# Kernel optimization log

Measured on AMD Instinct MI355X. Metric: run time of the kernel, lower is better.

Reference implementation:

```python
import jax, jax.numpy as jnp
import numpy as np

B, S, D = 4, 2048, 1024
H = 4096          # adapter hidden dim
E = 4             # number of adapters / experts


def setup_inputs() -> dict:
    key = jax.random.key(0)
    ks = jax.random.split(key, 7)
    sd = 1.0 / np.sqrt(D)
    sh = 1.0 / np.sqrt(H)
    return {
        "x":  jax.random.normal(ks[0], (B, S, D), dtype=jnp.float32),
        "Wr": jax.random.uniform(ks[1], (D, E), minval=-sd, maxval=sd, dtype=jnp.float32),
        "br": jax.random.uniform(ks[2], (E,), minval=-sd, maxval=sd, dtype=jnp.float32),
        "W1": jax.random.uniform(ks[3], (E, D, H), minval=-sd, maxval=sd, dtype=jnp.float32),
        "b1": jax.random.uniform(ks[4], (E, H), minval=-sd, maxval=sd, dtype=jnp.float32),
        "W2": jax.random.uniform(ks[5], (E, H, D), minval=-sh, maxval=sh, dtype=jnp.float32),
        "b2": jax.random.uniform(ks[6], (E, D), minval=-sh, maxval=sh, dtype=jnp.float32),
    }


def reference(x, Wr, br, W1, b1, W2, b2):
    # Flatten tokens: (N, D)
    xf = x.reshape(-1, D)
    N = xf.shape[0]

    # Top-1 router (route_type='none' -> router input is x itself)
    logits = xf @ Wr + br                      # (N, E)
    probs = jax.nn.softmax(logits, axis=-1)    # (N, E)
    gate_idx = jnp.argmax(probs, axis=-1)      # (N,) int
    gate_val = jnp.max(probs, axis=-1)         # (N,)

    # Run every expert adapter densely (E small), then select per token.
    h = jnp.einsum('nd,edh->enh', xf, W1) + b1[:, None, :]   # (E, N, H)
    h = jax.nn.silu(h)
    eo = jnp.einsum('enh,ehd->end', h, W2) + b2[:, None, :]  # (E, N, D)

    sel = eo[gate_idx, jnp.arange(N)]          # (N, D) per-token expert output
    out = sel * gate_val[:, None]              # is_scale_prob=True scaling
    return out.reshape(B, S, D)
```

## Files before the change

kernel.cpp:

```cpp
#include <hip/hip_runtime.h>

#define DN 8192
#define DD 1024
#define DH 4096
#define DE 4
#define SLOTS (DN + 512)

typedef unsigned short u16;
typedef float f32x4 __attribute__((ext_vector_type(4)));
typedef __bf16 bf16x8 __attribute__((ext_vector_type(8)));
typedef u16 u16x2 __attribute__((ext_vector_type(2)));
typedef u16 u16x4 __attribute__((ext_vector_type(4)));

__device__ __forceinline__ u16 f2b(float f) {
  union { float f; unsigned u; } v; v.f = f;
  return (u16)((v.u + 0x7FFFu + ((v.u >> 16) & 1u)) >> 16);
}

__device__ __forceinline__ void gl_lds16(const u16* g, u16* l) {
  __builtin_amdgcn_global_load_lds((const __attribute__((address_space(1))) void*)g,
                                   (__attribute__((address_space(3))) void*)l, 16, 0, 0);
}

__global__ __launch_bounds__(256) void router_k(const float* __restrict__ x,
    const float* __restrict__ Wr, const float* __restrict__ br,
    float* __restrict__ gval, int* __restrict__ gidx, int* __restrict__ gpos,
    int* __restrict__ counts, u16* __restrict__ xb)
{
  const int tid = blockIdx.x * 256 + threadIdx.x;
  const int n = tid >> 6, lane = tid & 63;
  const float* xr = x + (size_t)n * DD;
  double a0 = 0., a1 = 0., a2 = 0., a3 = 0.;
#pragma unroll
  for (int k = 0; k < DD / 64; ++k) {
    const int d = lane + k * 64;
    const float xv = xr[d];
    const f32x4 w = *(const f32x4*)&Wr[d * 4];
    a0 += (double)xv * w[0]; a1 += (double)xv * w[1];
    a2 += (double)xv * w[2]; a3 += (double)xv * w[3];
    xb[(size_t)n * DD + d] = f2b(xv);
  }
#pragma unroll
  for (int off = 32; off; off >>= 1) {
    a0 += __shfl_xor(a0, off);
    a1 += __shfl_xor(a1, off);
    a2 += __shfl_xor(a2, off);
    a3 += __shfl_xor(a3, off);
  }
  if (lane == 0) {
    const double l0 = a0 + br[0], l1 = a1 + br[1], l2 = a2 + br[2], l3 = a3 + br[3];
    int bi = 0; double bm = l0;
    if (l1 > bm) { bm = l1; bi = 1; }
    if (l2 > bm) { bm = l2; bi = 2; }
    if (l3 > bm) { bm = l3; bi = 3; }
    const float s = __expf((float)(l0 - bm)) + __expf((float)(l1 - bm)) +
                    __expf((float)(l2 - bm)) + __expf((float)(l3 - bm));
    gval[n] = 1.0f / s;
    gidx[n] = bi;
    gpos[n] = atomicAdd(&counts[bi], 1);
  }
}

__global__ void offsets_k(const int* __restrict__ counts, int* __restrict__ offs) {
  if (threadIdx.x == 0 && blockIdx.x == 0) {
    int o = 0;
#pragma unroll
    for (int e = 0; e < DE; ++e) { offs[e] = o; o += (counts[e] + 127) & ~127; }
    offs[DE] = o;
  }
}

__global__ __launch_bounds__(256) void scatter_k(const int* __restrict__ gidx,
    const int* __restrict__ gpos, const int* __restrict__ offs, int* __restrict__ tlist) {
  const int n = blockIdx.x * 256 + threadIdx.x;
  tlist[offs[gidx[n]] + gpos[n]] = n;
}

__global__ __launch_bounds__(256) void transpose_conv(const float* __restrict__ in,
    u16* __restrict__ out, int R, int C)
{
  __shared__ u16 t[64][66];
  const int r0 = blockIdx.x * 64, c0 = blockIdx.y * 64;
  const size_t mo = (size_t)blockIdx.z * R * C;
  const int tid = threadIdx.x;
  const int i = tid >> 4, j0 = (tid & 15) * 4;
#pragma unroll
  for (int k = 0; k < 4; ++k) {
    const int row = k * 16 + i;
    const f32x4 v = *(const f32x4*)&in[mo + (size_t)(r0 + row) * C + c0 + j0];
    u16x2 u01; u01[0] = f2b(v[0]); u01[1] = f2b(v[1]);
    u16x2 u23; u23[0] = f2b(v[2]); u23[1] = f2b(v[3]);
    *(u16x2*)&t[row][j0] = u01;
    *(u16x2*)&t[row][j0 + 2] = u23;
  }
  __syncthreads();
#pragma unroll
  for (int k = 0; k < 4; ++k) {
    const int p = k * 16 + i;
    u16x4 u;
    u[0] = t[j0 + 0][p]; u[1] = t[j0 + 1][p]; u[2] = t[j0 + 2][p]; u[3] = t[j0 + 3][p];
    *(u16x4*)&out[mo + (size_t)(c0 + p) * R + r0 + j0] = u;
  }
}

#define STAGE(ks, B) do { \
    gl_lds16(pa0 + (size_t)(ks) * 32, &As[B][wid][0][0]); \
    gl_lds16(pa1 + (size_t)(ks) * 32, &As[B][wid][64][0]); \
    gl_lds16(pb0 + (size_t)(ks) * 32, &Bs[B][wid][0][0]); \
    gl_lds16(pb1 + (size_t)(ks) * 32, &Bs[B][wid][64][0]); \
  } while (0)

#define COMPUTE(B) do { \
    bf16x8 af[4], bfv[4]; \
    _Pragma("unroll") \
    for (int m = 0; m < 4; ++m) af[m] = *(const bf16x8*)&As[B][fq][wr + m * 16 + fr][0]; \
    _Pragma("unroll") \
    for (int n = 0; n < 4; ++n) bfv[n] = *(const bf16x8*)&Bs[B][fq][wc + n * 16 + fr][0]; \
    _Pragma("unroll") \
    for (int m = 0; m < 4; ++m) \
      _Pragma("unroll") \
      for (int n = 0; n < 4; ++n) \
        acc[m][n] = __builtin_amdgcn_mfma_f32_16x16x32_bf16(af[m], bfv[n], acc[m][n], 0, 0, 0); \
  } while (0)

#define GITER(ks, CUR, NXT, NK) do { \
    if ((ks) + 1 < (NK)) { \
      STAGE((ks) + 1, NXT); \
      asm volatile("s_waitcnt vmcnt(4)" ::: "memory"); \
    } else { \
      asm volatile("s_waitcnt vmcnt(0)" ::: "memory"); \
    } \
    __builtin_amdgcn_s_barrier(); \
    __builtin_amdgcn_sched_barrier(0); \
    COMPUTE(CUR); \
    __builtin_amdgcn_sched_barrier(0); \
    __builtin_amdgcn_s_barrier(); \
  } while (0)

__global__ __launch_bounds__(256) void gemm1_k(const u16* __restrict__ xb,
    const u16* __restrict__ w1t, const float* __restrict__ b1,
    const int* __restrict__ tlist, const int* __restrict__ offs, u16* __restrict__ hb)
{
  __shared__ u16 As[2][4][128][8];
  __shared__ u16 Bs[2][4][128][8];
  const int row0 = blockIdx.x * 128;
  if (row0 >= offs[DE]) return;
  int e = 0;
  if (row0 >= offs[1]) e = 1;
  if (row0 >= offs[2]) e = 2;
  if (row0 >= offs[3]) e = 3;
  const int h0 = blockIdx.y * 128;
  const int tid = threadIdx.x;
  const int wid = tid >> 6, lane = tid & 63;

  int tA0 = tlist[row0 + lane];
  int tA1 = tlist[row0 + 64 + lane];
  if (tA0 < 0) tA0 = 0;
  if (tA1 < 0) tA1 = 0;
  const u16* pa0 = xb + (size_t)tA0 * DD + wid * 8;
  const u16* pa1 = xb + (size_t)tA1 * DD + wid * 8;
  const u16* pb0 = w1t + (size_t)e * DH * DD + (size_t)(h0 + lane) * DD + wid * 8;
  const u16* pb1 = w1t + (size_t)e * DH * DD + (size_t)(h0 + 64 + lane) * DD + wid * 8;

  const int wr = (wid >> 1) * 64, wc = (wid & 1) * 64;
  const int fr = lane & 15, fq = lane >> 4;

  f32x4 acc[4][4];
#pragma unroll
  for (int m = 0; m < 4; ++m)
#pragma unroll
    for (int n = 0; n < 4; ++n) acc[m][n] = (f32x4)(0.f);

  STAGE(0, 0);
#pragma unroll 1
  for (int ks = 0; ks < DD / 32; ks += 2) {
    GITER(ks, 0, 1, DD / 32);
    GITER(ks + 1, 1, 0, DD / 32);
  }

#pragma unroll
  for (int n = 0; n < 4; ++n) {
    const int h = h0 + wc + n * 16 + fr;
    const float bias = b1[(size_t)e * DH + h];
#pragma unroll
    for (int m = 0; m < 4; ++m) {
      const int r = row0 + wr + m * 16 + fq * 4;
      const f32x4 v = acc[m][n];
#pragma unroll
      for (int i = 0; i < 4; ++i) {
        const float xv = v[i] + bias;
        const float sv = xv / (1.f + __expf(-xv));
        hb[(size_t)(r + i) * DH + h] = f2b(sv);
      }
    }
  }
}

__global__ __launch_bounds__(256) void gemm2_k(const u16* __restrict__ hb,
    const u16* __restrict__ w2t, const int* __restrict__ tlist,
    const int* __restrict__ offs, float* __restrict__ out, float* __restrict__ p1)
{
  __shared__ u16 As[2][4][128][8];
  __shared__ u16 Bs[2][4][128][8];
  const int row0 = blockIdx.x * 128;
  if (row0 >= offs[DE]) return;
  int e = 0;
  if (row0 >= offs[1]) e = 1;
  if (row0 >= offs[2]) e = 2;
  if (row0 >= offs[3]) e = 3;
  const int d0 = blockIdx.y * 128;
  const int kb = blockIdx.z * (DH / 2);
  const int tid = threadIdx.x;
  const int wid = tid >> 6, lane = tid & 63;

  const u16* pa0 = hb + (size_t)(row0 + lane) * DH + kb + wid * 8;
  const u16* pa1 = hb + (size_t)(row0 + 64 + lane) * DH + kb + wid * 8;
  const u16* pb0 = w2t + (size_t)e * DD * DH + (size_t)(d0 + lane) * DH + kb + wid * 8;
  const u16* pb1 = w2t + (size_t)e * DD * DH + (size_t)(d0 + 64 + lane) * DH + kb + wid * 8;

  const int wr = (wid >> 1) * 64, wc = (wid & 1) * 64;
  const int fr = lane & 15, fq = lane >> 4;

  f32x4 acc[4][4];
#pragma unroll
  for (int m = 0; m < 4; ++m)
#pragma unroll
    for (int n = 0; n < 4; ++n) acc[m][n] = (f32x4)(0.f);

  STAGE(0, 0);
#pragma unroll 1
  for (int ks = 0; ks < DH / 2 / 32; ks += 2) {
    GITER(ks, 0, 1, DH / 2 / 32);
    GITER(ks + 1, 1, 0, DH / 2 / 32);
  }

  float* __restrict__ dst = (blockIdx.z == 0) ? out : p1;
  int tok[4][4];
#pragma unroll
  for (int m = 0; m < 4; ++m) {
    const int rb = row0 + wr + m * 16 + fq * 4;
#pragma unroll
    for (int i = 0; i < 4; ++i) tok[m][i] = tlist[rb + i];
  }
#pragma unroll
  for (int n = 0; n < 4; ++n) {
    const int d = d0 + wc + n * 16 + fr;
#pragma unroll
    for (int m = 0; m < 4; ++m)
#pragma unroll
      for (int i = 0; i < 4; ++i) {
        const int t = tok[m][i];
        if (t >= 0) dst[(size_t)t * DD + d] = acc[m][n][i];
      }
  }
}

__global__ __launch_bounds__(256) void reduce2_k(float* __restrict__ out,
    const float* __restrict__ p1, const float* __restrict__ b2,
    const int* __restrict__ gidx, const float* __restrict__ gval)
{
  const size_t idx = ((size_t)blockIdx.x * 256 + threadIdx.x) * 4;
  const int n = (int)(idx >> 10);
  const int d = (int)(idx & (DD - 1));
  const int e = gidx[n];
  const float g = gval[n];
  f32x4 a = *(f32x4*)&out[idx];
  const f32x4 b = *(const f32x4*)&p1[idx];
  const f32x4 bb = *(const f32x4*)&b2[(size_t)e * DD + d];
  f32x4 r;
#pragma unroll
  for (int j = 0; j < 4; ++j) r[j] = (a[j] + b[j] + bb[j]) * g;
  *(f32x4*)&out[idx] = r;
}

extern "C" void kernel_launch(void* const* d_in, const int* in_sizes, int n_in,
                              void* d_out, int out_size, void* d_ws, size_t ws_size,
                              hipStream_t stream) {
  const float* x  = (const float*)d_in[0];
  const float* Wr = (const float*)d_in[1];
  const float* br = (const float*)d_in[2];
  const float* W1 = (const float*)d_in[3];
  const float* b1 = (const float*)d_in[4];
  const float* W2 = (const float*)d_in[5];
  const float* b2 = (const float*)d_in[6];
  float* out = (float*)d_out;

  char* ws = (char*)d_ws;
  int*   counts = (int*)ws;
  int*   offs   = (int*)(ws + 256);
  float* gval   = (float*)(ws + 512);
  int*   gidx   = (int*)(ws + 512 + 32768);
  int*   gpos   = (int*)(ws + 512 + 65536);
  int*   tlist  = (int*)(ws + 512 + 98304);
  size_t off = 512 + 98304 + 34816;
  u16* xb  = (u16*)(ws + off);
  float* p1 = (float*)(ws + off);
  off += (size_t)DN * DD * 2;
  u16* w1t = (u16*)(ws + off); off += (size_t)DE * DH * DD * 2;
  u16* w2t = (u16*)(ws + off); off += (size_t)DE * DD * DH * 2;
  u16* hb  = (u16*)(ws + off);

  hipMemsetAsync(counts, 0, 256, stream);
  hipMemsetAsync(tlist, 0xFF, SLOTS * sizeof(int), stream);

  router_k<<<dim3(DN / 4), 256, 0, stream>>>(x, Wr, br, gval, gidx, gpos, counts, xb);
  offsets_k<<<dim3(1), 64, 0, stream>>>(counts, offs);
  scatter_k<<<dim3(DN / 256), 256, 0, stream>>>(gidx, gpos, offs, tlist);
  transpose_conv<<<dim3(DD / 64, DH / 64, DE), 256, 0, stream>>>(W1, w1t, DD, DH);
  transpose_conv<<<dim3(DH / 64, DD / 64, DE), 256, 0, stream>>>(W2, w2t, DH, DD);
  gemm1_k<<<dim3(DN / 128 + DE, DH / 128), 256, 0, stream>>>(xb, w1t, b1, tlist, offs, hb);
  gemm2_k<<<dim3(DN / 128 + DE, DD / 128, 2), 256, 0, stream>>>(hb, w2t, tlist, offs, out, p1);
  reduce2_k<<<dim3(DN * DD / 4 / 256), 256, 0, stream>>>(out, p1, b2, gidx, gval);
}
```

Measured before the change: 677.9 us.

## Enlarge grouped GEMM tiles to 256x256 with 512 threads and XCD-aware block remap

Both expert GEMMs move from 128x128 tiles on 256 threads to 256x256 tiles on 512 threads, with each wave holding a 128x64 accumulator. Expert segments are padded to 256 rows so each tile stays within one expert. The grid becomes 1-D and is remapped so consecutive workgroups land on the same XCD. The pipeline is restructured to issue the next stage's loads before compute, using one barrier per step instead of two, and MFMA issue is wrapped in setprio. The aim is more operand reuse per LDS load and less sync overhead. In exchange it costs more padded rows, higher register pressure from 128 accumulator floats per thread, and fewer workgroups per GEMM.

New measurement: 703.5 us. 3.8% more time.

```diff
diff --git a/kernel.cpp b/kernel.cpp
--- a/kernel.cpp
+++ b/kernel.cpp
@@ -4,7 +4,8 @@
 #define DD 1024
 #define DH 4096
 #define DE 4
-#define SLOTS (DN + 512)
+#define SLOTS (DN + DE * 256)
+#define RT (SLOTS / 256)
 
 typedef unsigned short u16;
 typedef float f32x4 __attribute__((ext_vector_type(4)));
@@ -65,7 +66,7 @@
   if (threadIdx.x == 0 && blockIdx.x == 0) {
     int o = 0;
 #pragma unroll
-    for (int e = 0; e < DE; ++e) { offs[e] = o; o += (counts[e] + 127) & ~127; }
+    for (int e = 0; e < DE; ++e) { offs[e] = o; o += (counts[e] + 255) & ~255; }
     offs[DE] = o;
   }
 }
@@ -103,87 +104,94 @@
   }
 }
 
-#define STAGE(ks, B) do { \
-    gl_lds16(pa0 + (size_t)(ks) * 32, &As[B][wid][0][0]); \
-    gl_lds16(pa1 + (size_t)(ks) * 32, &As[B][wid][64][0]); \
-    gl_lds16(pb0 + (size_t)(ks) * 32, &Bs[B][wid][0][0]); \
-    gl_lds16(pb1 + (size_t)(ks) * 32, &Bs[B][wid][64][0]); \
+#define STAGE(t, B) do { \
+    gl_lds16(pa0 + (size_t)(t) * 32, &As[B][kc][rb0][0]); \
+    gl_lds16(pa1 + (size_t)(t) * 32, &As[B][kc][rb0 + 64][0]); \
+    gl_lds16(pb0 + (size_t)(t) * 32, &Bs[B][kc][rb0][0]); \
+    gl_lds16(pb1 + (size_t)(t) * 32, &Bs[B][kc][rb0 + 64][0]); \
   } while (0)
 
 #define COMPUTE(B) do { \
-    bf16x8 af[4], bfv[4]; \
+    bf16x8 af[8], bfv[4]; \
     _Pragma("unroll") \
-    for (int m = 0; m < 4; ++m) af[m] = *(const bf16x8*)&As[B][fq][wr + m * 16 + fr][0]; \
+    for (int m = 0; m < 8; ++m) af[m] = *(const bf16x8*)&As[B][fq][wr + m * 16 + fr][0]; \
     _Pragma("unroll") \
     for (int n = 0; n < 4; ++n) bfv[n] = *(const bf16x8*)&Bs[B][fq][wc + n * 16 + fr][0]; \
+    __builtin_amdgcn_s_setprio(1); \
     _Pragma("unroll") \
-    for (int m = 0; m < 4; ++m) \
+    for (int m = 0; m < 8; ++m) \
       _Pragma("unroll") \
       for (int n = 0; n < 4; ++n) \
         acc[m][n] = __builtin_amdgcn_mfma_f32_16x16x32_bf16(af[m], bfv[n], acc[m][n], 0, 0, 0); \
+    __builtin_amdgcn_s_setprio(0); \
   } while (0)
 
-#define GITER(ks, CUR, NXT, NK) do { \
-    if ((ks) + 1 < (NK)) { \
-      STAGE((ks) + 1, NXT); \
-      asm volatile("s_waitcnt vmcnt(4)" ::: "memory"); \
-    } else { \
-      asm volatile("s_waitcnt vmcnt(0)" ::: "memory"); \
-    } \
+#define GI(t, CUR, NXT) do { \
+    STAGE((t) + 1, NXT); \
+    COMPUTE(CUR); \
+    __builtin_amdgcn_sched_barrier(0); \
+    asm volatile("s_waitcnt vmcnt(0)" ::: "memory"); \
     __builtin_amdgcn_s_barrier(); \
     __builtin_amdgcn_sched_barrier(0); \
-    COMPUTE(CUR); \
-    __builtin_amdgcn_sched_barrier(0); \
-    __builtin_amdgcn_s_barrier(); \
   } while (0)
 
-__global__ __launch_bounds__(256) void gemm1_k(const u16* __restrict__ xb,
+__global__ __launch_bounds__(512, 2) void gemm1_k(const u16* __restrict__ xb,
     const u16* __restrict__ w1t, const float* __restrict__ b1,
     const int* __restrict__ tlist, const int* __restrict__ offs, u16* __restrict__ hb)
 {
-  __shared__ u16 As[2][4][128][8];
-  __shared__ u16 Bs[2][4][128][8];
-  const int row0 = blockIdx.x * 128;
+  __shared__ u16 As[2][4][256][8];
+  __shared__ u16 Bs[2][4][256][8];
+  const int nwg = RT * (DH / 256);
+  const int bq = nwg >> 3;
+  const int wg = (blockIdx.x & 7) * bq + (blockIdx.x >> 3);
+  const int row0 = (wg % RT) * 256;
+  const int h0 = (wg / RT) * 256;
   if (row0 >= offs[DE]) return;
   int e = 0;
   if (row0 >= offs[1]) e = 1;
   if (row0 >= offs[2]) e = 2;
   if (row0 >= offs[3]) e = 3;
-  const int h0 = blockIdx.y * 128;
   const int tid = threadIdx.x;
   const int wid = tid >> 6, lane = tid & 63;
-
-  int tA0 = tlist[row0 + lane];
-  int tA1 = tlist[row0 + 64 + lane];
+  const int kc = wid >> 1, rb0 = (wid & 1) * 128;
+
+  int tA0 = tlist[row0 + rb0 + lane];
+  int tA1 = tlist[row0 + rb0 + 64 + lane];
   if (tA0 < 0) tA0 = 0;
   if (tA1 < 0) tA1 = 0;
-  const u16* pa0 = xb + (size_t)tA0 * DD + wid * 8;
-  const u16* pa1 = xb + (size_t)tA1 * DD + wid * 8;
-  const u16* pb0 = w1t + (size_t)e * DH * DD + (size_t)(h0 + lane) * DD + wid * 8;
-  const u16* pb1 = w1t + (size_t)e * DH * DD + (size_t)(h0 + 64 + lane) * DD + wid * 8;
-
-  const int wr = (wid >> 1) * 64, wc = (wid & 1) * 64;
+  const u16* pa0 = xb + (size_t)tA0 * DD + kc * 8;
+  const u16* pa1 = xb + (size_t)tA1 * DD + kc * 8;
+  const u16* pb0 = w1t + ((size_t)e * DH + h0 + rb0 + lane) * DD + kc * 8;
+  const u16* pb1 = pb0 + (size_t)64 * DD;
+
+  const int wr = (wid >> 2) * 128, wc = (wid & 3) * 64;
   const int fr = lane & 15, fq = lane >> 4;
 
-  f32x4 acc[4][4];
-#pragma unroll
-  for (int m = 0; m < 4; ++m)
+  f32x4 acc[8][4];
+#pragma unroll
+  for (int m = 0; m < 8; ++m)
 #pragma unroll
     for (int n = 0; n < 4; ++n) acc[m][n] = (f32x4)(0.f);
 
   STAGE(0, 0);
+  asm volatile("s_waitcnt vmcnt(0)" ::: "memory");
+  __builtin_amdgcn_s_barrier();
+  __builtin_amdgcn_sched_barrier(0);
+#define NK1 (DD / 32)
 #pragma unroll 1
-  for (int ks = 0; ks < DD / 32; ks += 2) {
-    GITER(ks, 0, 1, DD / 32);
-    GITER(ks + 1, 1, 0, DD / 32);
-  }
+  for (int ks = 0; ks < NK1 - 2; ks += 2) {
+    GI(ks, 0, 1);
+    GI(ks + 1, 1, 0);
+  }
+  GI(NK1 - 2, 0, 1);
+  COMPUTE(1);
 
 #pragma unroll
   for (int n = 0; n < 4; ++n) {
     const int h = h0 + wc + n * 16 + fr;
     const float bias = b1[(size_t)e * DH + h];
 #pragma unroll
-    for (int m = 0; m < 4; ++m) {
+    for (int m = 0; m < 8; ++m) {
       const int r = row0 + wr + m * 16 + fq * 4;
       const f32x4 v = acc[m][n];
 #pragma unroll
@@ -196,48 +204,59 @@
   }
 }
 
-__global__ __launch_bounds__(256) void gemm2_k(const u16* __restrict__ hb,
+__global__ __launch_bounds__(512, 2) void gemm2_k(const u16* __restrict__ hb,
     const u16* __restrict__ w2t, const int* __restrict__ tlist,
     const int* __restrict__ offs, float* __restrict__ out, float* __restrict__ p1)
 {
-  __shared__ u16 As[2][4][128][8];
-  __shared__ u16 Bs[2][4][128][8];
-  const int row0 = blockIdx.x * 128;
+  __shared__ u16 As[2][4][256][8];
+  __shared__ u16 Bs[2][4][256][8];
+  const int nwg = RT * (DD / 256) * 2;
+  const int bq = nwg >> 3;
+  const int wg = (blockIdx.x & 7) * bq + (blockIdx.x >> 3);
+  const int row0 = (wg % RT) * 256;
+  const int rest = wg / RT;
+  const int d0 = (rest & 3) * 256;
+  const int kb = (rest >> 2) * (DH / 2);
   if (row0 >= offs[DE]) return;
   int e = 0;
   if (row0 >= offs[1]) e = 1;
   if (row0 >= offs[2]) e = 2;
   if (row0 >= offs[3]) e = 3;
-  const int d0 = blockIdx.y * 128;
-  const int kb = blockIdx.z * (DH / 2);
   const int tid = threadIdx.x;
   const int wid = tid >> 6, lane = tid & 63;
-
-  const u16* pa0 = hb + (size_t)(row0 + lane) * DH + kb + wid * 8;
-  const u16* pa1 = hb + (size_t)(row0 + 64 + lane) * DH + kb + wid * 8;
-  const u16* pb0 = w2t + (size_t)e * DD * DH + (size_t)(d0 + lane) * DH + kb + wid * 8;
-  const u16* pb1 = w2t + (size_t)e * DD * DH + (size_t)(d0 + 64 + lane) * DH + kb + wid * 8;
-
-  const int wr = (wid >> 1) * 64, wc = (wid & 1) * 64;
+  const int kc = wid >> 1, rb0 = (wid & 1) * 128;
+
+  const u16* pa0 = hb + ((size_t)(row0 + rb0 + lane)) * DH + kb + kc * 8;
+  const u16* pa1 = pa0 + (size_t)64 * DH;
+  const u16* pb0 = w2t + ((size_t)e * DD + d0 + rb0 + lane) * DH + kb + kc * 8;
+  const u16* pb1 = pb0 + (size_t)64 * DH;
+
+  const int wr = (wid >> 2) * 128, wc = (wid & 3) * 64;
   const int fr = lane & 15, fq = lane >> 4;
 
-  f32x4 acc[4][4];
-#pragma unroll
-  for (int m = 0; m < 4; ++m)
+  f32x4 acc[8][4];
+#pragma unroll
+  for (int m = 0; m < 8; ++m)
 #pragma unroll
     for (int n = 0; n < 4; ++n) acc[m][n] = (f32x4)(0.f);
 
   STAGE(0, 0);
+  asm volatile("s_waitcnt vmcnt(0)" ::: "memory");
+  __builtin_amdgcn_s_barrier();
+  __builtin_amdgcn_sched_barrier(0);
+#define NK2 (DH / 2 / 32)
 #pragma unroll 1
-  for (int ks = 0; ks < DH / 2 / 32; ks += 2) {
-    GITER(ks, 0, 1, DH / 2 / 32);
-    GITER(ks + 1, 1, 0, DH / 2 / 32);
-  }
-
-  float* __restrict__ dst = (blockIdx.z == 0) ? out : p1;
-  int tok[4][4];
-#pragma unroll
-  for (int m = 0; m < 4; ++m) {
+  for (int ks = 0; ks < NK2 - 2; ks += 2) {
+    GI(ks, 0, 1);
+    GI(ks + 1, 1, 0);
+  }
+  GI(NK2 - 2, 0, 1);
+  COMPUTE(1);
+
+  float* __restrict__ dst = (kb == 0) ? out : p1;
+  int tok[8][4];
+#pragma unroll
+  for (int m = 0; m < 8; ++m) {
     const int rb = row0 + wr + m * 16 + fq * 4;
 #pragma unroll
     for (int i = 0; i < 4; ++i) tok[m][i] = tlist[rb + i];
@@ -246,7 +265,7 @@
   for (int n = 0; n < 4; ++n) {
     const int d = d0 + wc + n * 16 + fr;
 #pragma unroll
-    for (int m = 0; m < 4; ++m)
+    for (int m = 0; m < 8; ++m)
 #pragma unroll
       for (int i = 0; i < 4; ++i) {
         const int t = tok[m][i];
@@ -292,7 +311,7 @@
   int*   gidx   = (int*)(ws + 512 + 32768);
   int*   gpos   = (int*)(ws + 512 + 65536);
   int*   tlist  = (int*)(ws + 512 + 98304);
-  size_t off = 512 + 98304 + 34816;
+  size_t off = 512 + 98304 + 36864;
   u16* xb  = (u16*)(ws + off);
   float* p1 = (float*)(ws + off);
   off += (size_t)DN * DD * 2;
@@ -308,7 +327,7 @@
   scatter_k<<<dim3(DN / 256), 256, 0, stream>>>(gidx, gpos, offs, tlist);
   transpose_conv<<<dim3(DD / 64, DH / 64, DE), 256, 0, stream>>>(W1, w1t, DD, DH);
   transpose_conv<<<dim3(DH / 64, DD / 64, DE), 256, 0, stream>>>(W2, w2t, DH, DD);
-  gemm1_k<<<dim3(DN / 128 + DE, DH / 128), 256, 0, stream>>>(xb, w1t, b1, tlist, offs, hb);
-  gemm2_k<<<dim3(DN / 128 + DE, DD / 128, 2), 256, 0, stream>>>(hb, w2t, tlist, offs, out, p1);
+  gemm1_k<<<dim3(RT * (DH / 256)), 512, 0, stream>>>(xb, w1t, b1, tlist, offs, hb);
+  gemm2_k<<<dim3(RT * (DD / 256) * 2), 512, 0, stream>>>(hb, w2t, tlist, offs, out, p1);
   reduce2_k<<<dim3(DN * DD / 4 / 256), 256, 0, stream>>>(out, p1, b2, gidx, gval);
 }
```
